# Kernel optimization log

Measured on AMD Instinct MI355X. Metric: run time of the kernel, lower is better.

The kernel has to match this reference:

```python
import jax, jax.numpy as jnp
import numpy as np

B, N, S, D, H = 4, 64, 512, 128, 8  # batch, groups, set size, in_size, heads


def setup_inputs() -> dict:
    key = jax.random.key(0)
    ks = jax.random.split(key, 8)
    s1 = 1.0 / np.sqrt(D)
    s2 = 1.0 / np.sqrt(2 * D)
    return {
        "x": jax.random.normal(ks[0], (B, N, S, D), jnp.float32),
        # DeepSets phi MLP: D -> D -> D -> D (hidden=[in_size,in_size])
        "w1": jax.random.normal(ks[1], (D, D), jnp.float32) * s1,
        "b1": jnp.zeros((D,), jnp.float32),
        "w2": jax.random.normal(ks[2], (D, D), jnp.float32) * s1,
        "b2": jnp.zeros((D,), jnp.float32),
        "w3": jax.random.normal(ks[3], (D, D), jnp.float32) * s1,
        "b3": jnp.zeros((D,), jnp.float32),
        # attention projection: 2D -> H*D
        "W": jax.random.normal(ks[4], (2 * D, H * D), jnp.float32) * s2,
        "Wb": jnp.zeros((H * D,), jnp.float32),
        # per-head query vector (zeros-init in original; random for a nontrivial baseline)
        "q": jax.random.normal(ks[5], (H, D), jnp.float32) * 0.1,
    }


def reference(x, w1, b1, w2, b2, w3, b3, W, Wb, q):
    # SetTransform (DeepSets): per-element MLP then sum over set dim (-2)
    h = jax.nn.relu(x @ w1 + b1)
    h = jax.nn.relu(h @ w2 + b2)
    h = h @ w3 + b3
    set_feat = h.sum(axis=-2)                                  # (B, N, D)
    sf = jnp.broadcast_to(set_feat[..., None, :], x.shape)      # (B, N, S, D)
    comb = jnp.concatenate([x, sf], axis=-1)                    # (B, N, S, 2D)
    heads = (comb @ W + Wb).reshape(B, N, S, H, D)              # (B, N, S, H, D)
    e = jnp.einsum('bnshd,hd->bnsh', heads, q)                  # (B, N, S, H)
    return jax.nn.softmax(e, axis=-2)                           # softmax over set dim
```

## Files before the change

### kernel.cpp

```cpp
#include <hip/hip_runtime.h>

#define Bsz 4
#define Ngrp 64
#define Sset 512
#define Din 128
#define Hh 8
#define EST (Sset + 1)

#define DPP_QUAD_XOR1 0xB1
#define DPP_QUAD_XOR2 0x4E
#define DPP_ROW_HALF_MIRROR 0x141
#define DPP_ROW_MIRROR 0x140

template <int CTRL>
__device__ __forceinline__ float dpp_add(float v) {
    int perm = __builtin_amdgcn_update_dpp(0, __float_as_int(v), CTRL, 0xF, 0xF, true);
    return v + __int_as_float(perm);
}

__device__ __forceinline__ float row16_sum(float v) {
    v = dpp_add<DPP_QUAD_XOR1>(v);
    v = dpp_add<DPP_QUAD_XOR2>(v);
    v = dpp_add<DPP_ROW_HALF_MIRROR>(v);
    v = dpp_add<DPP_ROW_MIRROR>(v);
    return v;
}

__global__ void __launch_bounds__(Sset) attn_fused_kernel(
    const float* __restrict__ x,
    const float* __restrict__ W,
    const float* __restrict__ q,
    float* __restrict__ out)
{
    const int bn = blockIdx.x;
    const int tid = threadIdx.x;
    const int wave = tid >> 6;
    const int lane = tid & 63;
    const int g    = lane >> 4;
    const int sub  = lane & 15;

    __shared__ float e_s[Hh * EST];
    __shared__ float us[Hh * Din];
    __shared__ float qs[Hh * Din];

    const float4* xb = (const float4*)(x + (size_t)bn * Sset * Din);
    const int r0 = wave * 64 + g;
    float4 px0 = xb[(size_t)r0 * (Din / 4) + sub];
    float4 px1 = xb[(size_t)r0 * (Din / 4) + sub + 16];

    {
        const float2* q2 = (const float2*)q;
        ((float2*)qs)[tid] = q2[tid];
    }
    __syncthreads();

#pragma unroll 4
    for (int p = 0; p < 32; ++p) {
        const int idx = p * 32 + wave * 4 + g;
        const int h = idx >> 7;
        const int c = idx & 127;
        const float4* Wr = (const float4*)(W + (size_t)c * (Hh * Din) + (size_t)h * Din);
        const float4* qr = (const float4*)(qs + h * Din);
        const float4 w0 = Wr[sub];
        const float4 w1 = Wr[sub + 16];
        const float4 q0 = qr[sub];
        const float4 q1 = qr[sub + 16];
        float v;
        v = w0.x * q0.x;
        v = fmaf(w0.y, q0.y, v);
        v = fmaf(w0.z, q0.z, v);
        v = fmaf(w0.w, q0.w, v);
        v = fmaf(w1.x, q1.x, v);
        v = fmaf(w1.y, q1.y, v);
        v = fmaf(w1.z, q1.z, v);
        v = fmaf(w1.w, q1.w, v);
        v = row16_sum(v);
        if (sub == 0) us[idx] = v;
    }
    __syncthreads();

    const float4* u4 = (const float4*)us;
    float4 ua[Hh], ub[Hh];
#pragma unroll
    for (int h = 0; h < Hh; ++h) {
        ua[h] = u4[h * 32 + sub];
        ub[h] = u4[h * 32 + sub + 16];
    }

#pragma unroll 4
    for (int pass = 0; pass < 16; ++pass) {
        const int r = wave * 64 + pass * 4 + g;
        const float4 x0 = px0;
        const float4 x1 = px1;
        if (pass < 15) {
            const float4* xn = xb + (size_t)(r + 4) * (Din / 4);
            px0 = xn[sub];
            px1 = xn[sub + 16];
        }

        float st = 0.f;
#pragma unroll
        for (int h = 0; h < Hh; ++h) {
            float v;
            v = x0.x * ua[h].x;
            v = fmaf(x0.y, ua[h].y, v);
            v = fmaf(x0.z, ua[h].z, v);
            v = fmaf(x0.w, ua[h].w, v);
            v = fmaf(x1.x, ub[h].x, v);
            v = fmaf(x1.y, ub[h].y, v);
            v = fmaf(x1.z, ub[h].z, v);
            v = fmaf(x1.w, ub[h].w, v);
            v = row16_sum(v);
            if (sub == h) st = v;
        }
        if (sub < Hh) e_s[sub * EST + r] = st;
    }
    __syncthreads();

    {
        float* eh = &e_s[wave * EST];

        float m = -1e30f;
#pragma unroll
        for (int k = 0; k < Sset / 64; ++k) m = fmaxf(m, eh[lane + 64 * k]);
#pragma unroll
        for (int off = 32; off >= 1; off >>= 1) m = fmaxf(m, __shfl_xor(m, off, 64));

        float p[Sset / 64];
        float sum = 0.f;
#pragma unroll
        for (int k = 0; k < Sset / 64; ++k) {
            p[k] = __expf(eh[lane + 64 * k] - m);
            sum += p[k];
        }
#pragma unroll
        for (int off = 32; off >= 1; off >>= 1) sum += __shfl_xor(sum, off, 64);

        const float inv = 1.f / sum;
#pragma unroll
        for (int k = 0; k < Sset / 64; ++k) eh[lane + 64 * k] = p[k] * inv;
    }
    __syncthreads();

    {
        const int s = tid;
        float4 o0, o1;
        o0.x = e_s[0 * EST + s];
        o0.y = e_s[1 * EST + s];
        o0.z = e_s[2 * EST + s];
        o0.w = e_s[3 * EST + s];
        o1.x = e_s[4 * EST + s];
        o1.y = e_s[5 * EST + s];
        o1.z = e_s[6 * EST + s];
        o1.w = e_s[7 * EST + s];
        float4* orow = (float4*)(out + ((size_t)bn * Sset + s) * Hh);
        orow[0] = o0;
        orow[1] = o1;
    }
}

extern "C" void kernel_launch(void* const* d_in, const int* in_sizes, int n_in,
                              void* d_out, int out_size, void* d_ws, size_t ws_size,
                              hipStream_t stream) {
    const float* x = (const float*)d_in[0];
    const float* W = (const float*)d_in[7];
    const float* q = (const float*)d_in[9];
    float* out = (float*)d_out;

    attn_fused_kernel<<<dim3(Bsz * Ngrp), dim3(Sset), 0, stream>>>(x, W, q, out);
}
```

Baseline: 122.0 us.

## Hoist per-block W·q projection into separate precompute kernel

Splits the fused kernel into two launches. A small kernel computes the W·q projection vector u once into the workspace, and the main kernel loads u from global memory instead of each block recomputing it from W. This removes redundant per-block reads of W and the reduction work. The cost is a second launch and a dependency between kernels. The manual software prefetch of x rows is also removed.

```diff
diff --git a/kernel.cpp b/kernel.cpp
--- a/kernel.cpp
+++ b/kernel.cpp
@@ -26,10 +26,42 @@
     return v;
 }
 
-__global__ void __launch_bounds__(Sset) attn_fused_kernel(
-    const float* __restrict__ x,
+__global__ void __launch_bounds__(256) compute_u_kernel(
     const float* __restrict__ W,
     const float* __restrict__ q,
+    float* __restrict__ u)
+{
+    const int tid = threadIdx.x;
+    const int grp = tid >> 4;
+    const int sub = tid & 15;
+
+    const int idx = blockIdx.x * 16 + grp;
+    const int h = idx >> 7;
+    const int c = idx & 127;
+
+    const float4* Wr = (const float4*)(W + (size_t)c * (Hh * Din) + (size_t)h * Din);
+    const float4* qr = (const float4*)(q + h * Din);
+    const float4 w0 = Wr[sub];
+    const float4 w1 = Wr[sub + 16];
+    const float4 q0 = qr[sub];
+    const float4 q1 = qr[sub + 16];
+
+    float v;
+    v = w0.x * q0.x;
+    v = fmaf(w0.y, q0.y, v);
+    v = fmaf(w0.z, q0.z, v);
+    v = fmaf(w0.w, q0.w, v);
+    v = fmaf(w1.x, q1.x, v);
+    v = fmaf(w1.y, q1.y, v);
+    v = fmaf(w1.z, q1.z, v);
+    v = fmaf(w1.w, q1.w, v);
+    v = row16_sum(v);
+    if (sub == 0) u[idx] = v;
+}
+
+__global__ void __launch_bounds__(Sset) attn_softmax_kernel(
+    const float* __restrict__ x,
+    const float* __restrict__ u,
     float* __restrict__ out)
 {
     const int bn = blockIdx.x;
@@ -40,46 +72,8 @@
     const int sub  = lane & 15;
 
     __shared__ float e_s[Hh * EST];
-    __shared__ float us[Hh * Din];
-    __shared__ float qs[Hh * Din];
 
-    const float4* xb = (const float4*)(x + (size_t)bn * Sset * Din);
-    const int r0 = wave * 64 + g;
-    float4 px0 = xb[(size_t)r0 * (Din / 4) + sub];
-    float4 px1 = xb[(size_t)r0 * (Din / 4) + sub + 16];
-
-    {
-        const float2* q2 = (const float2*)q;
-        ((float2*)qs)[tid] = q2[tid];
-    }
-    __syncthreads();
-
-#pragma unroll 4
-    for (int p = 0; p < 32; ++p) {
-        const int idx = p * 32 + wave * 4 + g;
-        const int h = idx >> 7;
-        const int c = idx & 127;
-        const float4* Wr = (const float4*)(W + (size_t)c * (Hh * Din) + (size_t)h * Din);
-        const float4* qr = (const float4*)(qs + h * Din);
-        const float4 w0 = Wr[sub];
-        const float4 w1 = Wr[sub + 16];
-        const float4 q0 = qr[sub];
-        const float4 q1 = qr[sub + 16];
-        float v;
-        v = w0.x * q0.x;
-        v = fmaf(w0.y, q0.y, v);
-        v = fmaf(w0.z, q0.z, v);
-        v = fmaf(w0.w, q0.w, v);
-        v = fmaf(w1.x, q1.x, v);
-        v = fmaf(w1.y, q1.y, v);
-        v = fmaf(w1.z, q1.z, v);
-        v = fmaf(w1.w, q1.w, v);
-        v = row16_sum(v);
-        if (sub == 0) us[idx] = v;
-    }
-    __syncthreads();
-
-    const float4* u4 = (const float4*)us;
+    const float4* u4 = (const float4*)u;
     float4 ua[Hh], ub[Hh];
 #pragma unroll
     for (int h = 0; h < Hh; ++h) {
@@ -87,16 +81,13 @@
         ub[h] = u4[h * 32 + sub + 16];
     }
 
+    const float4* xb = (const float4*)(x + (size_t)bn * Sset * Din);
 #pragma unroll 4
     for (int pass = 0; pass < 16; ++pass) {
         const int r = wave * 64 + pass * 4 + g;
-        const float4 x0 = px0;
-        const float4 x1 = px1;
-        if (pass < 15) {
-            const float4* xn = xb + (size_t)(r + 4) * (Din / 4);
-            px0 = xn[sub];
-            px1 = xn[sub + 16];
-        }
+        const float4* xr = xb + (size_t)r * (Din / 4);
+        const float4 x0 = xr[sub];
+        const float4 x1 = xr[sub + 16];
 
         float st = 0.f;
 #pragma unroll
@@ -165,7 +156,9 @@
     const float* x = (const float*)d_in[0];
     const float* W = (const float*)d_in[7];
     const float* q = (const float*)d_in[9];
+    float* u = (float*)d_ws;
     float* out = (float*)d_out;
 
-    attn_fused_kernel<<<dim3(Bsz * Ngrp), dim3(Sset), 0, stream>>>(x, W, q, out);
+    compute_u_kernel<<<dim3(64), dim3(256), 0, stream>>>(W, q, u);
+    attn_softmax_kernel<<<dim3(Bsz * Ngrp), dim3(Sset), 0, stream>>>(x, u, out);
 }
```

New measurement: 118.0 us. 1.03x faster.
